# Kernel tuning notes

Hardware: AMD Instinct MI355X
Metric: run time of the kernel (lower is better)

## Reference

```python
import jax, jax.numpy as jnp
import numpy as np

HC = 6.62607015e-34 * 2.99792458e8  # Planck*c in J*m


def lattice_to_primitive(lattice):
    """[a,b,c,alpha,beta,gamma] -> 3x3 primitive basis (columns e1,e2,e3)."""
    a, b, c = lattice[0], lattice[1], lattice[2]
    cal, cbe = jnp.cos(lattice[3]), jnp.cos(lattice[4])
    cga, sga = jnp.cos(lattice[5]), jnp.sin(lattice[5])
    e3y = (cal - cbe * cga) / sga
    e3z = jnp.sqrt(jnp.maximum(1.0 - cbe * cbe - e3y * e3y, 1e-12))
    o = jnp.zeros((), lattice.dtype)
    prim = jnp.stack([
        jnp.stack([a, b * cga, c * cbe]),
        jnp.stack([o, b * sga, c * e3y]),
        jnp.stack([o, o, c * e3z]),
    ])
    return prim


def primitive_to_reciprocal(prim):
    # e*_i = (e_j x e_k) / V  <=>  inv(prim).T for 3x3 basis-as-columns
    return jnp.linalg.inv(prim).T


def omega_to_rot(angle):
    """3 elementary rotation angles -> Rx(t1) @ Ry(t2) @ Rz(t3)."""
    c, s = jnp.cos(angle), jnp.sin(angle)
    o = jnp.zeros((), angle.dtype)
    l = jnp.ones((), angle.dtype)
    rx = jnp.stack([jnp.stack([l, o, o]), jnp.stack([o, c[0], -s[0]]), jnp.stack([o, s[0], c[0]])])
    ry = jnp.stack([jnp.stack([c[1], o, s[1]]), jnp.stack([o, l, o]), jnp.stack([-s[1], o, c[1]])])
    rz = jnp.stack([jnp.stack([c[2], -s[2], o]), jnp.stack([s[2], c[2], o]), jnp.stack([o, o, l])])
    return rx @ ry @ rz


def _np_primitive(lattice):
    a, b, c, al, be, ga = [float(v) for v in lattice]
    cal, cbe, cga, sga = np.cos(al), np.cos(be), np.cos(ga), np.sin(ga)
    e3y = (cal - cbe * cga) / sga
    e3z = np.sqrt(max(1.0 - cbe * cbe - e3y * e3y, 1e-12))
    return np.array([[a, b * cga, c * cbe], [0.0, b * sga, c * e3y], [0.0, 0.0, c * e3z]])


def setup_inputs() -> dict:
    key = jax.random.key(0)
    lattice_np = np.array([3.6e-10, 3.6e-10, 3.6e-10, np.pi / 2, np.pi / 2, np.pi / 2], np.float64)
    e_min = 5e3 * 1.602176634e-19   # 5 keV in J
    e_max = 25e3 * 1.602176634e-19  # 25 keV in J

    # select_hkl: all nonzero hkl inside the Ewald ball ||B @ hkl|| <= 2*e_max/(h*c)
    recip_np = np.linalg.inv(_np_primitive(lattice_np)).T
    q_max = 2.0 * e_max / HC
    n_max = int(np.ceil(q_max * lattice_np[:3].max())) + 1
    grid = np.arange(-n_max, n_max + 1)
    hkl_all = np.stack(np.meshgrid(grid, grid, grid, indexing="ij"), axis=-1).reshape(-1, 3)
    q_norm = np.linalg.norm(hkl_all @ recip_np.T, axis=1)
    hkl = hkl_all[(q_norm <= q_max) & (q_norm > 0.0)].astype(np.int32)  # (~12k, 3)

    n_exp = 5000
    uq_exp = jax.random.normal(key, (n_exp, 3), dtype=jnp.float32)
    uq_exp = uq_exp / jnp.linalg.norm(uq_exp, axis=1, keepdims=True)

    return {
        "lattice": jnp.asarray(lattice_np, jnp.float32),
        "angle": jnp.zeros(3, jnp.float32),
        "uq_exp": uq_exp,
        "hkl": jnp.asarray(hkl),
        "phi_max": jnp.float32(0.5 * np.pi / 180.0),
        "e_min": jnp.float32(e_min),
    }


def reference(lattice, angle, uq_exp, hkl, phi_max, e_min):
    # rotate reciprocal lattice into lab frame
    reciprocal = primitive_to_reciprocal(lattice_to_primitive(lattice))
    rot = omega_to_rot(angle)
    reciprocal_lab = rot @ reciprocal                      # (3,3)

    # hkl -> diffraction vectors, unit uq and energies
    q = hkl.astype(lattice.dtype) @ reciprocal_lab.T       # (m,3)
    q_norm = jnp.linalg.norm(q, axis=1)                    # (m,)
    uq_theo = q / q_norm[:, None]                          # (m,3)
    sin_theta = jnp.abs(uq_theo[:, 2])                     # incident beam along z
    energy = HC * q_norm / (2.0 * jnp.maximum(sin_theta, 1e-9))
    keep = energy >= e_min                                 # (m,) energy filter mask

    # continuous matching rate: soft count of exp rays close to a kept theo ray
    cosang = jnp.clip(uq_exp @ uq_theo.T, -1.0 + 1e-6, 1.0 - 1e-6)  # (n,m)
    phi = jnp.arccos(cosang)
    phi = jnp.where(keep[None, :], phi, jnp.pi)            # masked rays -> max distance
    phi_min = jnp.min(phi, axis=1)                         # (n,)
    rate = jnp.mean(jnp.exp(-0.5 * (phi_min / phi_max) ** 2))
    return rate
```

## Files before the change

kernel.cpp:

```cpp
#include <hip/hip_runtime.h>
#include <math.h>

#define HCF 1.98644586e-25f

constexpr int BLOCK = 256;
constexpr int RPT   = 4;
constexpr int RAYS_PER_BLOCK = BLOCK * RPT;

__global__ __launch_bounds__(BLOCK) void refiner_maxdot_kernel(
    const float* __restrict__ lattice, const float* __restrict__ angle,
    const float* __restrict__ uq_exp,  const int* __restrict__ hkl,
    const float* __restrict__ e_min_p,
    unsigned* __restrict__ maxenc, int n, int m, int nchunks)
{
    __shared__ float4 s_uq[BLOCK];
    const int tid   = threadIdx.x;
    const int chunk = blockIdx.x % nchunks;
    const int rg    = blockIdx.x / nchunks;

    const float a = lattice[0], b = lattice[1], cc = lattice[2];
    const float cal = cosf(lattice[3]), cbe = cosf(lattice[4]);
    const float cga = cosf(lattice[5]), sga = sinf(lattice[5]);
    const float e3y = (cal - cbe * cga) / sga;
    const float e3z = sqrtf(fmaxf(1.0f - cbe * cbe - e3y * e3y, 1e-12f));
    const float p01 = b * cga, p02 = cc * cbe, p11 = b * sga, p12 = cc * e3y, p22 = cc * e3z;
    const float i00 = 1.0f / a, i11 = 1.0f / p11, i22 = 1.0f / p22;
    const float i01 = -p01 * (i00 * i11);
    const float i12 = -p12 * (i11 * i22);
    const float i02 = (p01 * p12 - p02 * p11) * (i00 * i11 * i22);
    const float c0 = cosf(angle[0]), s0 = sinf(angle[0]);
    const float c1 = cosf(angle[1]), s1 = sinf(angle[1]);
    const float c2 = cosf(angle[2]), s2 = sinf(angle[2]);
    const float M00 = c1 * c2,               M01 = -c1 * s2,              M02 = s1;
    const float M10 = c0 * s2 + s0 * s1 * c2, M11 = c0 * c2 - s0 * s1 * s2, M12 = -s0 * c1;
    const float M20 = s0 * s2 - c0 * s1 * c2, M21 = s0 * c2 + c0 * s1 * s2, M22 = c0 * c1;
    const float B00 = M00 * i00 + M01 * i01 + M02 * i02;
    const float B01 = M01 * i11 + M02 * i12;
    const float B02 = M02 * i22;
    const float B10 = M10 * i00 + M11 * i01 + M12 * i02;
    const float B11 = M11 * i11 + M12 * i12;
    const float B12 = M12 * i22;
    const float B20 = M20 * i00 + M21 * i01 + M22 * i02;
    const float B21 = M21 * i11 + M22 * i12;
    const float B22 = M22 * i22;

    const int ti = chunk * BLOCK + tid;
    float4 v = make_float4(0.f, 0.f, 0.f, 0.f);
    if (ti < m) {
        const float h0 = (float)hkl[3 * ti + 0];
        const float h1 = (float)hkl[3 * ti + 1];
        const float h2 = (float)hkl[3 * ti + 2];
        const float qx = B00 * h0 + B01 * h1 + B02 * h2;
        const float qy = B10 * h0 + B11 * h1 + B12 * h2;
        const float qz = B20 * h0 + B21 * h1 + B22 * h2;
        const float qn = sqrtf(qx * qx + qy * qy + qz * qz);
        const float inv = 1.0f / qn;
        const float ux = qx * inv, uy = qy * inv, uz = qz * inv;
        const float st = fabsf(uz);
        const float energy = HCF * qn / (2.0f * fmaxf(st, 1e-9f));
        if (energy >= e_min_p[0]) v = make_float4(ux, uy, uz, 0.f);
    }
    s_uq[tid] = v;
    __syncthreads();

    float rx[RPT], ry[RPT], rz[RPT], mx[RPT];
    bool valid[RPT];
#pragma unroll
    for (int i = 0; i < RPT; ++i) {
        const int ray = rg * RAYS_PER_BLOCK + i * BLOCK + tid;
        valid[i] = (ray < n);
        float x = 0.f, y = 0.f, z = 0.f;
        if (valid[i]) { x = uq_exp[3 * ray]; y = uq_exp[3 * ray + 1]; z = uq_exp[3 * ray + 2]; }
        rx[i] = x; ry[i] = y; rz[i] = z;
        mx[i] = 0.f;
    }

#pragma unroll 4
    for (int j = 0; j < BLOCK; ++j) {
        const float4 t = s_uq[j];
#pragma unroll
        for (int i = 0; i < RPT; ++i) {
            const float d = rx[i] * t.x + ry[i] * t.y + rz[i] * t.z;
            mx[i] = fmaxf(mx[i], d);
        }
    }

#pragma unroll
    for (int i = 0; i < RPT; ++i) {
        if (valid[i]) {
            const int ray = rg * RAYS_PER_BLOCK + i * BLOCK + tid;
            atomicMax(&maxenc[ray], __float_as_uint(mx[i]));
        }
    }
}

__global__ __launch_bounds__(BLOCK) void refiner_finalize_kernel(
    const unsigned* __restrict__ maxenc, const float* __restrict__ phi_max_p,
    float* __restrict__ out, int n)
{
    const int i = blockIdx.x * BLOCK + threadIdx.x;
    float w = 0.f;
    if (i < n) {
        float c = __uint_as_float(maxenc[i]);
        c = fminf(c, 1.0f - 1e-6f);
        const float phi = acosf(c);
        const float t = phi / phi_max_p[0];
        w = expf(-0.5f * t * t);
    }
#pragma unroll
    for (int off = 32; off > 0; off >>= 1) w += __shfl_down(w, off, 64);
    __shared__ float s[BLOCK / 64];
    const int lane = threadIdx.x & 63, wv = threadIdx.x >> 6;
    if (lane == 0) s[wv] = w;
    __syncthreads();
    if (threadIdx.x == 0) {
        float tot = 0.f;
#pragma unroll
        for (int k = 0; k < BLOCK / 64; ++k) tot += s[k];
        atomicAdd(out, tot / (float)n);
    }
}

extern "C" void kernel_launch(void* const* d_in, const int* in_sizes, int n_in,
                              void* d_out, int out_size, void* d_ws, size_t ws_size,
                              hipStream_t stream) {
    const float* lattice = (const float*)d_in[0];
    const float* angle   = (const float*)d_in[1];
    const float* uq_exp  = (const float*)d_in[2];
    const int*   hkl     = (const int*)d_in[3];
    const float* phi_max = (const float*)d_in[4];
    const float* e_min   = (const float*)d_in[5];
    const int n = in_sizes[2] / 3;
    const int m = in_sizes[3] / 3;

    unsigned* maxenc = (unsigned*)d_ws;

    hipMemsetAsync(maxenc, 0, (size_t)n * sizeof(unsigned), stream);
    hipMemsetAsync(d_out, 0, sizeof(float), stream);

    const int nchunks = (m + BLOCK - 1) / BLOCK;
    const int nrg     = (n + RAYS_PER_BLOCK - 1) / RAYS_PER_BLOCK;
    refiner_maxdot_kernel<<<dim3(nrg * nchunks), dim3(BLOCK), 0, stream>>>(
        lattice, angle, uq_exp, hkl, e_min, maxenc, n, m, nchunks);
    refiner_finalize_kernel<<<dim3((n + BLOCK - 1) / BLOCK), dim3(BLOCK), 0, stream>>>(
        maxenc, phi_max, (float*)d_out, n);
}
```

Measured before the change: 84.87 us.

## Fuse finalize into maxdot kernel via last-block counter and halve rays per thread

Merges the finalize reduction into the main kernel: each block increments a global counter after its atomicMax updates, and the last block to finish computes the Gaussian-weighted mean over all rays. This removes one kernel launch and one memset, but the whole final reduction now runs in a single block. RPT drops from 4 to 2, which doubles the grid and the hkl/energy recomputation per block, and the inner loop unroll goes from 4 to 8. The single-block tail over n rays may serialize if n is large.

Result: slower. 113.0 us (+33.1%).

```diff
diff --git a/kernel.cpp b/kernel.cpp
--- a/kernel.cpp
+++ b/kernel.cpp
@@ -4,14 +4,15 @@
 #define HCF 1.98644586e-25f
 
 constexpr int BLOCK = 256;
-constexpr int RPT   = 4;
+constexpr int RPT   = 2;
 constexpr int RAYS_PER_BLOCK = BLOCK * RPT;
 
-__global__ __launch_bounds__(BLOCK) void refiner_maxdot_kernel(
+__global__ __launch_bounds__(BLOCK) void refiner_fused_kernel(
     const float* __restrict__ lattice, const float* __restrict__ angle,
     const float* __restrict__ uq_exp,  const int* __restrict__ hkl,
-    const float* __restrict__ e_min_p,
-    unsigned* __restrict__ maxenc, int n, int m, int nchunks)
+    const float* __restrict__ phi_max_p, const float* __restrict__ e_min_p,
+    unsigned* __restrict__ maxenc, unsigned* __restrict__ counter,
+    float* __restrict__ out, int n, int m, int nchunks)
 {
     __shared__ float4 s_uq[BLOCK];
     const int tid   = threadIdx.x;
@@ -31,7 +32,7 @@
     const float c0 = cosf(angle[0]), s0 = sinf(angle[0]);
     const float c1 = cosf(angle[1]), s1 = sinf(angle[1]);
     const float c2 = cosf(angle[2]), s2 = sinf(angle[2]);
-    const float M00 = c1 * c2,               M01 = -c1 * s2,              M02 = s1;
+    const float M00 = c1 * c2,                M01 = -c1 * s2,               M02 = s1;
     const float M10 = c0 * s2 + s0 * s1 * c2, M11 = c0 * c2 - s0 * s1 * s2, M12 = -s0 * c1;
     const float M20 = s0 * s2 - c0 * s1 * c2, M21 = s0 * c2 + c0 * s1 * s2, M22 = c0 * c1;
     const float B00 = M00 * i00 + M01 * i01 + M02 * i02;
@@ -64,18 +65,16 @@
     __syncthreads();
 
     float rx[RPT], ry[RPT], rz[RPT], mx[RPT];
-    bool valid[RPT];
 #pragma unroll
     for (int i = 0; i < RPT; ++i) {
         const int ray = rg * RAYS_PER_BLOCK + i * BLOCK + tid;
-        valid[i] = (ray < n);
         float x = 0.f, y = 0.f, z = 0.f;
-        if (valid[i]) { x = uq_exp[3 * ray]; y = uq_exp[3 * ray + 1]; z = uq_exp[3 * ray + 2]; }
+        if (ray < n) { x = uq_exp[3 * ray]; y = uq_exp[3 * ray + 1]; z = uq_exp[3 * ray + 2]; }
         rx[i] = x; ry[i] = y; rz[i] = z;
         mx[i] = 0.f;
     }
 
-#pragma unroll 4
+#pragma unroll 8
     for (int j = 0; j < BLOCK; ++j) {
         const float4 t = s_uq[j];
 #pragma unroll
@@ -87,37 +86,39 @@
 
 #pragma unroll
     for (int i = 0; i < RPT; ++i) {
-        if (valid[i]) {
-            const int ray = rg * RAYS_PER_BLOCK + i * BLOCK + tid;
+        const int ray = rg * RAYS_PER_BLOCK + i * BLOCK + tid;
+        if (ray < n) {
             atomicMax(&maxenc[ray], __float_as_uint(mx[i]));
         }
     }
-}
 
-__global__ __launch_bounds__(BLOCK) void refiner_finalize_kernel(
-    const unsigned* __restrict__ maxenc, const float* __restrict__ phi_max_p,
-    float* __restrict__ out, int n)
-{
-    const int i = blockIdx.x * BLOCK + threadIdx.x;
-    float w = 0.f;
-    if (i < n) {
-        float c = __uint_as_float(maxenc[i]);
-        c = fminf(c, 1.0f - 1e-6f);
-        const float phi = acosf(c);
-        const float t = phi / phi_max_p[0];
-        w = expf(-0.5f * t * t);
+    __shared__ bool s_last;
+    __threadfence();
+    if (tid == 0) {
+        const unsigned c = atomicAdd(counter, 1u);
+        s_last = (c == (unsigned)(gridDim.x - 1));
+    }
+    __syncthreads();
+    if (!s_last) return;
+
+    const float inv_pm = 1.0f / phi_max_p[0];
+    float acc = 0.f;
+    for (int i = tid; i < n; i += BLOCK) {
+        const unsigned u = atomicMax(&maxenc[i], 0u);
+        const float c = fminf(__uint_as_float(u), 1.0f - 1e-6f);
+        const float t = acosf(c) * inv_pm;
+        acc += expf(-0.5f * t * t);
     }
 #pragma unroll
-    for (int off = 32; off > 0; off >>= 1) w += __shfl_down(w, off, 64);
-    __shared__ float s[BLOCK / 64];
-    const int lane = threadIdx.x & 63, wv = threadIdx.x >> 6;
-    if (lane == 0) s[wv] = w;
+    for (int off = 32; off > 0; off >>= 1) acc += __shfl_down(acc, off, 64);
+    __shared__ float s_red[BLOCK / 64];
+    if ((tid & 63) == 0) s_red[tid >> 6] = acc;
     __syncthreads();
-    if (threadIdx.x == 0) {
+    if (tid == 0) {
         float tot = 0.f;
 #pragma unroll
-        for (int k = 0; k < BLOCK / 64; ++k) tot += s[k];
-        atomicAdd(out, tot / (float)n);
+        for (int k = 0; k < BLOCK / 64; ++k) tot += s_red[k];
+        out[0] = tot / (float)n;
     }
 }
 
@@ -133,15 +134,14 @@
     const int n = in_sizes[2] / 3;
     const int m = in_sizes[3] / 3;
 
-    unsigned* maxenc = (unsigned*)d_ws;
+    unsigned* maxenc  = (unsigned*)d_ws;
+    unsigned* counter = maxenc + n;
 
-    hipMemsetAsync(maxenc, 0, (size_t)n * sizeof(unsigned), stream);
-    hipMemsetAsync(d_out, 0, sizeof(float), stream);
+    hipMemsetAsync(d_ws, 0, (size_t)(n + 1) * sizeof(unsigned), stream);
 
     const int nchunks = (m + BLOCK - 1) / BLOCK;
     const int nrg     = (n + RAYS_PER_BLOCK - 1) / RAYS_PER_BLOCK;
-    refiner_maxdot_kernel<<<dim3(nrg * nchunks), dim3(BLOCK), 0, stream>>>(
-        lattice, angle, uq_exp, hkl, e_min, maxenc, n, m, nchunks);
-    refiner_finalize_kernel<<<dim3((n + BLOCK - 1) / BLOCK), dim3(BLOCK), 0, stream>>>(
-        maxenc, phi_max, (float*)d_out, n);
+    refiner_fused_kernel<<<dim3(nrg * nchunks), dim3(BLOCK), 0, stream>>>(
+        lattice, angle, uq_exp, hkl, phi_max, e_min,
+        maxenc, counter, (float*)d_out, n, m, nchunks);
 }
```

## Split into theo precompute, G-way max partials, and two-stage reduction without atomics

Applied to the files above, without the earlier changes.

Precomputes the normalised, energy-filtered theoretical ray vectors once in a separate kernel instead of recomputing the lattice and rotation setup in every block. The max-dot kernel now splits the theoretical rays into a fixed 48 groups, reads them straight from global memory (uniform broadcast loads) and writes per-group partial maxima, which removes the atomicMax traffic and both memsets. A weight kernel reduces the partials, applies acos and exp, and writes per-block sums, and a final single-block kernel sums them deterministically. The cost is four launches instead of two and a larger partial buffer, and fewer rays per thread (2 instead of 4) lowers register reuse per loaded theo vector.

Result: slower. 101.2 us (+19.2%).

```diff
diff --git a/kernel.cpp b/kernel.cpp
--- a/kernel.cpp
+++ b/kernel.cpp
@@ -4,49 +4,45 @@
 #define HCF 1.98644586e-25f
 
 constexpr int BLOCK = 256;
-constexpr int RPT   = 4;
+constexpr int RPT   = 2;
 constexpr int RAYS_PER_BLOCK = BLOCK * RPT;
+constexpr int G     = 48;
 
-__global__ __launch_bounds__(BLOCK) void refiner_maxdot_kernel(
+__global__ __launch_bounds__(256) void theo_kernel(
     const float* __restrict__ lattice, const float* __restrict__ angle,
-    const float* __restrict__ uq_exp,  const int* __restrict__ hkl,
-    const float* __restrict__ e_min_p,
-    unsigned* __restrict__ maxenc, int n, int m, int nchunks)
+    const int* __restrict__ hkl, const float* __restrict__ e_min_p,
+    float4* __restrict__ theo, int m, int m_pad)
 {
-    __shared__ float4 s_uq[BLOCK];
-    const int tid   = threadIdx.x;
-    const int chunk = blockIdx.x % nchunks;
-    const int rg    = blockIdx.x / nchunks;
-
-    const float a = lattice[0], b = lattice[1], cc = lattice[2];
-    const float cal = cosf(lattice[3]), cbe = cosf(lattice[4]);
-    const float cga = cosf(lattice[5]), sga = sinf(lattice[5]);
-    const float e3y = (cal - cbe * cga) / sga;
-    const float e3z = sqrtf(fmaxf(1.0f - cbe * cbe - e3y * e3y, 1e-12f));
-    const float p01 = b * cga, p02 = cc * cbe, p11 = b * sga, p12 = cc * e3y, p22 = cc * e3z;
-    const float i00 = 1.0f / a, i11 = 1.0f / p11, i22 = 1.0f / p22;
-    const float i01 = -p01 * (i00 * i11);
-    const float i12 = -p12 * (i11 * i22);
-    const float i02 = (p01 * p12 - p02 * p11) * (i00 * i11 * i22);
-    const float c0 = cosf(angle[0]), s0 = sinf(angle[0]);
-    const float c1 = cosf(angle[1]), s1 = sinf(angle[1]);
-    const float c2 = cosf(angle[2]), s2 = sinf(angle[2]);
-    const float M00 = c1 * c2,               M01 = -c1 * s2,              M02 = s1;
-    const float M10 = c0 * s2 + s0 * s1 * c2, M11 = c0 * c2 - s0 * s1 * s2, M12 = -s0 * c1;
-    const float M20 = s0 * s2 - c0 * s1 * c2, M21 = s0 * c2 + c0 * s1 * s2, M22 = c0 * c1;
-    const float B00 = M00 * i00 + M01 * i01 + M02 * i02;
-    const float B01 = M01 * i11 + M02 * i12;
-    const float B02 = M02 * i22;
-    const float B10 = M10 * i00 + M11 * i01 + M12 * i02;
-    const float B11 = M11 * i11 + M12 * i12;
-    const float B12 = M12 * i22;
-    const float B20 = M20 * i00 + M21 * i01 + M22 * i02;
-    const float B21 = M21 * i11 + M22 * i12;
-    const float B22 = M22 * i22;
-
-    const int ti = chunk * BLOCK + tid;
+    const int ti = blockIdx.x * 256 + threadIdx.x;
+    if (ti >= m_pad) return;
     float4 v = make_float4(0.f, 0.f, 0.f, 0.f);
     if (ti < m) {
+        const float a = lattice[0], b = lattice[1], cc = lattice[2];
+        const float cal = cosf(lattice[3]), cbe = cosf(lattice[4]);
+        const float cga = cosf(lattice[5]), sga = sinf(lattice[5]);
+        const float e3y = (cal - cbe * cga) / sga;
+        const float e3z = sqrtf(fmaxf(1.0f - cbe * cbe - e3y * e3y, 1e-12f));
+        const float p01 = b * cga, p02 = cc * cbe, p11 = b * sga, p12 = cc * e3y, p22 = cc * e3z;
+        const float i00 = 1.0f / a, i11 = 1.0f / p11, i22 = 1.0f / p22;
+        const float i01 = -p01 * (i00 * i11);
+        const float i12 = -p12 * (i11 * i22);
+        const float i02 = (p01 * p12 - p02 * p11) * (i00 * i11 * i22);
+        const float c0 = cosf(angle[0]), s0 = sinf(angle[0]);
+        const float c1 = cosf(angle[1]), s1 = sinf(angle[1]);
+        const float c2 = cosf(angle[2]), s2 = sinf(angle[2]);
+        const float M00 = c1 * c2,                M01 = -c1 * s2,               M02 = s1;
+        const float M10 = c0 * s2 + s0 * s1 * c2, M11 = c0 * c2 - s0 * s1 * s2, M12 = -s0 * c1;
+        const float M20 = s0 * s2 - c0 * s1 * c2, M21 = s0 * c2 + c0 * s1 * s2, M22 = c0 * c1;
+        const float B00 = M00 * i00 + M01 * i01 + M02 * i02;
+        const float B01 = M01 * i11 + M02 * i12;
+        const float B02 = M02 * i22;
+        const float B10 = M10 * i00 + M11 * i01 + M12 * i02;
+        const float B11 = M11 * i11 + M12 * i12;
+        const float B12 = M12 * i22;
+        const float B20 = M20 * i00 + M21 * i01 + M22 * i02;
+        const float B21 = M21 * i11 + M22 * i12;
+        const float B22 = M22 * i22;
+
         const float h0 = (float)hkl[3 * ti + 0];
         const float h1 = (float)hkl[3 * ti + 1];
         const float h2 = (float)hkl[3 * ti + 2];
@@ -56,28 +52,34 @@
         const float qn = sqrtf(qx * qx + qy * qy + qz * qz);
         const float inv = 1.0f / qn;
         const float ux = qx * inv, uy = qy * inv, uz = qz * inv;
-        const float st = fabsf(uz);
-        const float energy = HCF * qn / (2.0f * fmaxf(st, 1e-9f));
+        const float energy = HCF * qn / (2.0f * fmaxf(fabsf(uz), 1e-9f));
         if (energy >= e_min_p[0]) v = make_float4(ux, uy, uz, 0.f);
     }
-    s_uq[tid] = v;
-    __syncthreads();
+    theo[ti] = v;
+}
+
+__global__ __launch_bounds__(BLOCK) void maxdot_kernel(
+    const float* __restrict__ uq_exp, const float4* __restrict__ theo,
+    float* __restrict__ part, int n, int n_pad, int cpg, int nrg)
+{
+    const int tid = threadIdx.x;
+    const int g   = blockIdx.x / nrg;
+    const int rg  = blockIdx.x % nrg;
 
     float rx[RPT], ry[RPT], rz[RPT], mx[RPT];
-    bool valid[RPT];
 #pragma unroll
     for (int i = 0; i < RPT; ++i) {
         const int ray = rg * RAYS_PER_BLOCK + i * BLOCK + tid;
-        valid[i] = (ray < n);
         float x = 0.f, y = 0.f, z = 0.f;
-        if (valid[i]) { x = uq_exp[3 * ray]; y = uq_exp[3 * ray + 1]; z = uq_exp[3 * ray + 2]; }
+        if (ray < n) { x = uq_exp[3 * ray]; y = uq_exp[3 * ray + 1]; z = uq_exp[3 * ray + 2]; }
         rx[i] = x; ry[i] = y; rz[i] = z;
         mx[i] = 0.f;
     }
 
+    const float4* __restrict__ th = theo + (size_t)g * cpg;
 #pragma unroll 4
-    for (int j = 0; j < BLOCK; ++j) {
-        const float4 t = s_uq[j];
+    for (int j = 0; j < cpg; ++j) {
+        const float4 t = th[j];
 #pragma unroll
         for (int i = 0; i < RPT; ++i) {
             const float d = rx[i] * t.x + ry[i] * t.y + rz[i] * t.z;
@@ -87,38 +89,43 @@
 
 #pragma unroll
     for (int i = 0; i < RPT; ++i) {
-        if (valid[i]) {
-            const int ray = rg * RAYS_PER_BLOCK + i * BLOCK + tid;
-            atomicMax(&maxenc[ray], __float_as_uint(mx[i]));
-        }
+        const int ray = rg * RAYS_PER_BLOCK + i * BLOCK + tid;
+        part[(size_t)g * n_pad + ray] = mx[i];
     }
 }
 
-__global__ __launch_bounds__(BLOCK) void refiner_finalize_kernel(
-    const unsigned* __restrict__ maxenc, const float* __restrict__ phi_max_p,
-    float* __restrict__ out, int n)
+__global__ __launch_bounds__(256) void weight_kernel(
+    const float* __restrict__ part, const float* __restrict__ phi_max_p,
+    float* __restrict__ bsums, int n, int n_pad)
 {
-    const int i = blockIdx.x * BLOCK + threadIdx.x;
+    const int tid = threadIdx.x;
+    const int ray = blockIdx.x * 256 + tid;
     float w = 0.f;
-    if (i < n) {
-        float c = __uint_as_float(maxenc[i]);
-        c = fminf(c, 1.0f - 1e-6f);
-        const float phi = acosf(c);
-        const float t = phi / phi_max_p[0];
+    if (ray < n) {
+        float mx = part[ray];
+#pragma unroll 4
+        for (int g = 1; g < G; ++g) mx = fmaxf(mx, part[(size_t)g * n_pad + ray]);
+        const float c = fminf(mx, 1.0f - 1e-6f);
+        const float t = acosf(c) / phi_max_p[0];
         w = expf(-0.5f * t * t);
     }
 #pragma unroll
     for (int off = 32; off > 0; off >>= 1) w += __shfl_down(w, off, 64);
-    __shared__ float s[BLOCK / 64];
-    const int lane = threadIdx.x & 63, wv = threadIdx.x >> 6;
-    if (lane == 0) s[wv] = w;
+    __shared__ float s_red[4];
+    if ((tid & 63) == 0) s_red[tid >> 6] = w;
     __syncthreads();
-    if (threadIdx.x == 0) {
-        float tot = 0.f;
+    if (tid == 0) bsums[blockIdx.x] = s_red[0] + s_red[1] + s_red[2] + s_red[3];
+}
+
+__global__ __launch_bounds__(64) void final_kernel(
+    const float* __restrict__ bsums, float* __restrict__ out, int nb, int n)
+{
+    const int t = threadIdx.x;
+    float s = 0.f;
+    for (int i = t; i < nb; i += 64) s += bsums[i];
 #pragma unroll
-        for (int k = 0; k < BLOCK / 64; ++k) tot += s[k];
-        atomicAdd(out, tot / (float)n);
-    }
+    for (int off = 32; off > 0; off >>= 1) s += __shfl_down(s, off, 64);
+    if (t == 0) out[0] = s / (float)n;
 }
 
 extern "C" void kernel_launch(void* const* d_in, const int* in_sizes, int n_in,
@@ -133,15 +140,21 @@
     const int n = in_sizes[2] / 3;
     const int m = in_sizes[3] / 3;
 
-    unsigned* maxenc = (unsigned*)d_ws;
+    const int cpg   = (((m + G - 1) / G) + 3) & ~3;
+    const int m_pad = cpg * G;
+    const int nrg   = (n + RAYS_PER_BLOCK - 1) / RAYS_PER_BLOCK;
+    const int n_pad = nrg * RAYS_PER_BLOCK;
+    const int nbC1  = (n + 255) / 256;
 
-    hipMemsetAsync(maxenc, 0, (size_t)n * sizeof(unsigned), stream);
-    hipMemsetAsync(d_out, 0, sizeof(float), stream);
+    float4* theo  = (float4*)d_ws;
+    float*  part  = (float*)((char*)d_ws + (size_t)m_pad * sizeof(float4));
+    float*  bsums = part + (size_t)G * n_pad;
 
-    const int nchunks = (m + BLOCK - 1) / BLOCK;
-    const int nrg     = (n + RAYS_PER_BLOCK - 1) / RAYS_PER_BLOCK;
-    refiner_maxdot_kernel<<<dim3(nrg * nchunks), dim3(BLOCK), 0, stream>>>(
-        lattice, angle, uq_exp, hkl, e_min, maxenc, n, m, nchunks);
-    refiner_finalize_kernel<<<dim3((n + BLOCK - 1) / BLOCK), dim3(BLOCK), 0, stream>>>(
-        maxenc, phi_max, (float*)d_out, n);
+    theo_kernel<<<dim3((m_pad + 255) / 256), dim3(256), 0, stream>>>(
+        lattice, angle, hkl, e_min, theo, m, m_pad);
+    maxdot_kernel<<<dim3(G * nrg), dim3(BLOCK), 0, stream>>>(
+        uq_exp, theo, part, n, n_pad, cpg, nrg);
+    weight_kernel<<<dim3(nbC1), dim3(256), 0, stream>>>(
+        part, phi_max, bsums, n, n_pad);
+    final_kernel<<<dim3(1), dim3(64), 0, stream>>>(bsums, (float*)d_out, nbC1, n);
 }
```

## Replace atomicMax with per-chunk partial maxima and drop memset launches

Applied to the files above, without the earlier changes.

Instead of atomicMax into a memset-initialised per-ray buffer, each block writes its per-ray maxima into a chunk-indexed partial array. The finalize kernel reduces across chunks before computing the weights. The output is zeroed inside the first kernel, which removes both memset calls, and the hkl chunk size is halved to create more blocks. The cost is a larger workspace and a serial loop over chunks in the finalize kernel. Zeroing out inside the first kernel relies on kernel ordering on the stream before the second kernel's atomicAdd.

After: 85.21 us. About the same (+0.4%).

```diff
diff --git a/kernel.cpp b/kernel.cpp
--- a/kernel.cpp
+++ b/kernel.cpp
@@ -6,77 +6,80 @@
 constexpr int BLOCK = 256;
 constexpr int RPT   = 4;
 constexpr int RAYS_PER_BLOCK = BLOCK * RPT;
+constexpr int CHUNK = 128;
 
-__global__ __launch_bounds__(BLOCK) void refiner_maxdot_kernel(
+__global__ __launch_bounds__(BLOCK) void maxdot_kernel(
     const float* __restrict__ lattice, const float* __restrict__ angle,
     const float* __restrict__ uq_exp,  const int* __restrict__ hkl,
     const float* __restrict__ e_min_p,
-    unsigned* __restrict__ maxenc, int n, int m, int nchunks)
+    float* __restrict__ part, float* __restrict__ out,
+    int n, int n_pad, int m, int nchunks)
 {
-    __shared__ float4 s_uq[BLOCK];
+    __shared__ float4 s_uq[CHUNK];
     const int tid   = threadIdx.x;
     const int chunk = blockIdx.x % nchunks;
     const int rg    = blockIdx.x / nchunks;
 
-    const float a = lattice[0], b = lattice[1], cc = lattice[2];
-    const float cal = cosf(lattice[3]), cbe = cosf(lattice[4]);
-    const float cga = cosf(lattice[5]), sga = sinf(lattice[5]);
-    const float e3y = (cal - cbe * cga) / sga;
-    const float e3z = sqrtf(fmaxf(1.0f - cbe * cbe - e3y * e3y, 1e-12f));
-    const float p01 = b * cga, p02 = cc * cbe, p11 = b * sga, p12 = cc * e3y, p22 = cc * e3z;
-    const float i00 = 1.0f / a, i11 = 1.0f / p11, i22 = 1.0f / p22;
-    const float i01 = -p01 * (i00 * i11);
-    const float i12 = -p12 * (i11 * i22);
-    const float i02 = (p01 * p12 - p02 * p11) * (i00 * i11 * i22);
-    const float c0 = cosf(angle[0]), s0 = sinf(angle[0]);
-    const float c1 = cosf(angle[1]), s1 = sinf(angle[1]);
-    const float c2 = cosf(angle[2]), s2 = sinf(angle[2]);
-    const float M00 = c1 * c2,               M01 = -c1 * s2,              M02 = s1;
-    const float M10 = c0 * s2 + s0 * s1 * c2, M11 = c0 * c2 - s0 * s1 * s2, M12 = -s0 * c1;
-    const float M20 = s0 * s2 - c0 * s1 * c2, M21 = s0 * c2 + c0 * s1 * s2, M22 = c0 * c1;
-    const float B00 = M00 * i00 + M01 * i01 + M02 * i02;
-    const float B01 = M01 * i11 + M02 * i12;
-    const float B02 = M02 * i22;
-    const float B10 = M10 * i00 + M11 * i01 + M12 * i02;
-    const float B11 = M11 * i11 + M12 * i12;
-    const float B12 = M12 * i22;
-    const float B20 = M20 * i00 + M21 * i01 + M22 * i02;
-    const float B21 = M21 * i11 + M22 * i12;
-    const float B22 = M22 * i22;
+    if (blockIdx.x == 0 && tid == 0) out[0] = 0.0f;
 
-    const int ti = chunk * BLOCK + tid;
-    float4 v = make_float4(0.f, 0.f, 0.f, 0.f);
-    if (ti < m) {
-        const float h0 = (float)hkl[3 * ti + 0];
-        const float h1 = (float)hkl[3 * ti + 1];
-        const float h2 = (float)hkl[3 * ti + 2];
-        const float qx = B00 * h0 + B01 * h1 + B02 * h2;
-        const float qy = B10 * h0 + B11 * h1 + B12 * h2;
-        const float qz = B20 * h0 + B21 * h1 + B22 * h2;
-        const float qn = sqrtf(qx * qx + qy * qy + qz * qz);
-        const float inv = 1.0f / qn;
-        const float ux = qx * inv, uy = qy * inv, uz = qz * inv;
-        const float st = fabsf(uz);
-        const float energy = HCF * qn / (2.0f * fmaxf(st, 1e-9f));
-        if (energy >= e_min_p[0]) v = make_float4(ux, uy, uz, 0.f);
+    if (tid < CHUNK) {
+        const float a = lattice[0], b = lattice[1], cc = lattice[2];
+        const float cal = cosf(lattice[3]), cbe = cosf(lattice[4]);
+        const float cga = cosf(lattice[5]), sga = sinf(lattice[5]);
+        const float e3y = (cal - cbe * cga) / sga;
+        const float e3z = sqrtf(fmaxf(1.0f - cbe * cbe - e3y * e3y, 1e-12f));
+        const float p01 = b * cga, p02 = cc * cbe, p11 = b * sga, p12 = cc * e3y, p22 = cc * e3z;
+        const float i00 = 1.0f / a, i11 = 1.0f / p11, i22 = 1.0f / p22;
+        const float i01 = -p01 * (i00 * i11);
+        const float i12 = -p12 * (i11 * i22);
+        const float i02 = (p01 * p12 - p02 * p11) * (i00 * i11 * i22);
+        const float c0 = cosf(angle[0]), s0 = sinf(angle[0]);
+        const float c1 = cosf(angle[1]), s1 = sinf(angle[1]);
+        const float c2 = cosf(angle[2]), s2 = sinf(angle[2]);
+        const float M00 = c1 * c2,                M01 = -c1 * s2,               M02 = s1;
+        const float M10 = c0 * s2 + s0 * s1 * c2, M11 = c0 * c2 - s0 * s1 * s2, M12 = -s0 * c1;
+        const float M20 = s0 * s2 - c0 * s1 * c2, M21 = s0 * c2 + c0 * s1 * s2, M22 = c0 * c1;
+        const float B00 = M00 * i00 + M01 * i01 + M02 * i02;
+        const float B01 = M01 * i11 + M02 * i12;
+        const float B02 = M02 * i22;
+        const float B10 = M10 * i00 + M11 * i01 + M12 * i02;
+        const float B11 = M11 * i11 + M12 * i12;
+        const float B12 = M12 * i22;
+        const float B20 = M20 * i00 + M21 * i01 + M22 * i02;
+        const float B21 = M21 * i11 + M22 * i12;
+        const float B22 = M22 * i22;
+
+        const int ti = chunk * CHUNK + tid;
+        float4 v = make_float4(0.f, 0.f, 0.f, 0.f);
+        if (ti < m) {
+            const float h0 = (float)hkl[3 * ti + 0];
+            const float h1 = (float)hkl[3 * ti + 1];
+            const float h2 = (float)hkl[3 * ti + 2];
+            const float qx = B00 * h0 + B01 * h1 + B02 * h2;
+            const float qy = B10 * h0 + B11 * h1 + B12 * h2;
+            const float qz = B20 * h0 + B21 * h1 + B22 * h2;
+            const float qn = sqrtf(qx * qx + qy * qy + qz * qz);
+            const float inv = 1.0f / qn;
+            const float ux = qx * inv, uy = qy * inv, uz = qz * inv;
+            const float energy = HCF * qn / (2.0f * fmaxf(fabsf(uz), 1e-9f));
+            if (energy >= e_min_p[0]) v = make_float4(ux, uy, uz, 0.f);
+        }
+        s_uq[tid] = v;
     }
-    s_uq[tid] = v;
     __syncthreads();
 
     float rx[RPT], ry[RPT], rz[RPT], mx[RPT];
-    bool valid[RPT];
 #pragma unroll
     for (int i = 0; i < RPT; ++i) {
         const int ray = rg * RAYS_PER_BLOCK + i * BLOCK + tid;
-        valid[i] = (ray < n);
         float x = 0.f, y = 0.f, z = 0.f;
-        if (valid[i]) { x = uq_exp[3 * ray]; y = uq_exp[3 * ray + 1]; z = uq_exp[3 * ray + 2]; }
+        if (ray < n) { x = uq_exp[3 * ray]; y = uq_exp[3 * ray + 1]; z = uq_exp[3 * ray + 2]; }
         rx[i] = x; ry[i] = y; rz[i] = z;
         mx[i] = 0.f;
     }
 
 #pragma unroll 4
-    for (int j = 0; j < BLOCK; ++j) {
+    for (int j = 0; j < CHUNK; ++j) {
         const float4 t = s_uq[j];
 #pragma unroll
         for (int i = 0; i < RPT; ++i) {
@@ -87,36 +90,33 @@
 
 #pragma unroll
     for (int i = 0; i < RPT; ++i) {
-        if (valid[i]) {
-            const int ray = rg * RAYS_PER_BLOCK + i * BLOCK + tid;
-            atomicMax(&maxenc[ray], __float_as_uint(mx[i]));
-        }
+        const int ray = rg * RAYS_PER_BLOCK + i * BLOCK + tid;
+        part[(size_t)chunk * n_pad + ray] = mx[i];
     }
 }
 
-__global__ __launch_bounds__(BLOCK) void refiner_finalize_kernel(
-    const unsigned* __restrict__ maxenc, const float* __restrict__ phi_max_p,
-    float* __restrict__ out, int n)
+__global__ __launch_bounds__(256) void weight_kernel(
+    const float* __restrict__ part, const float* __restrict__ phi_max_p,
+    float* __restrict__ out, int n, int n_pad, int nchunks)
 {
-    const int i = blockIdx.x * BLOCK + threadIdx.x;
+    const int tid = threadIdx.x;
+    const int ray = blockIdx.x * 256 + tid;
     float w = 0.f;
-    if (i < n) {
-        float c = __uint_as_float(maxenc[i]);
-        c = fminf(c, 1.0f - 1e-6f);
-        const float phi = acosf(c);
-        const float t = phi / phi_max_p[0];
+    if (ray < n) {
+        float mx = part[ray];
+#pragma unroll 4
+        for (int c = 1; c < nchunks; ++c) mx = fmaxf(mx, part[(size_t)c * n_pad + ray]);
+        const float cv = fminf(mx, 1.0f - 1e-6f);
+        const float t = acosf(cv) / phi_max_p[0];
         w = expf(-0.5f * t * t);
     }
 #pragma unroll
     for (int off = 32; off > 0; off >>= 1) w += __shfl_down(w, off, 64);
-    __shared__ float s[BLOCK / 64];
-    const int lane = threadIdx.x & 63, wv = threadIdx.x >> 6;
-    if (lane == 0) s[wv] = w;
+    __shared__ float s_red[4];
+    if ((tid & 63) == 0) s_red[tid >> 6] = w;
     __syncthreads();
-    if (threadIdx.x == 0) {
-        float tot = 0.f;
-#pragma unroll
-        for (int k = 0; k < BLOCK / 64; ++k) tot += s[k];
+    if (tid == 0) {
+        const float tot = s_red[0] + s_red[1] + s_red[2] + s_red[3];
         atomicAdd(out, tot / (float)n);
     }
 }
@@ -133,15 +133,14 @@
     const int n = in_sizes[2] / 3;
     const int m = in_sizes[3] / 3;
 
-    unsigned* maxenc = (unsigned*)d_ws;
+    const int nchunks = (m + CHUNK - 1) / CHUNK;
+    const int nrg     = (n + RAYS_PER_BLOCK - 1) / RAYS_PER_BLOCK;
+    const int n_pad   = nrg * RAYS_PER_BLOCK;
 
-    hipMemsetAsync(maxenc, 0, (size_t)n * sizeof(unsigned), stream);
-    hipMemsetAsync(d_out, 0, sizeof(float), stream);
+    float* part = (float*)d_ws;
 
-    const int nchunks = (m + BLOCK - 1) / BLOCK;
-    const int nrg     = (n + RAYS_PER_BLOCK - 1) / RAYS_PER_BLOCK;
-    refiner_maxdot_kernel<<<dim3(nrg * nchunks), dim3(BLOCK), 0, stream>>>(
-        lattice, angle, uq_exp, hkl, e_min, maxenc, n, m, nchunks);
-    refiner_finalize_kernel<<<dim3((n + BLOCK - 1) / BLOCK), dim3(BLOCK), 0, stream>>>(
-        maxenc, phi_max, (float*)d_out, n);
+    maxdot_kernel<<<dim3(nchunks * nrg), dim3(BLOCK), 0, stream>>>(
+        lattice, angle, uq_exp, hkl, e_min, part, (float*)d_out, n, n_pad, m, nchunks);
+    weight_kernel<<<dim3((n + 255) / 256), dim3(256), 0, stream>>>(
+        part, phi_max, (float*)d_out, n, n_pad, nchunks);
 }
```
